# Performance work log

Hardware: AMD Instinct MI355X
Metric: run time of the kernel (lower is better)

## Reference

```python
import jax, jax.numpy as jnp
import numpy as np

# PyTorch LSTM gate order: i, f, g, o. Biases b_ih+b_hh combined into one b.

def _lstm(x, Wih, Whh, b, reverse=False):
    # x: [T, B, D] time-major; Wih: [4H, D]; Whh: [4H, H]; b: [4H]
    H = Whh.shape[1]
    B = x.shape[1]
    xi = jnp.einsum('tbd,gd->tbg', x, Wih) + b  # precompute input projection over all timesteps
    def step(carry, xt):
        h, c = carry
        z = xt + h @ Whh.T
        i, f, g, o = jnp.split(z, 4, axis=-1)
        c = jax.nn.sigmoid(f) * c + jax.nn.sigmoid(i) * jnp.tanh(g)
        h = jax.nn.sigmoid(o) * jnp.tanh(c)
        return (h, c), h
    h0 = jnp.zeros((B, H), x.dtype)
    _, hs = jax.lax.scan(step, (h0, h0), xi, reverse=reverse)
    return hs  # [T, B, H], aligned with input time indices


def _bidir(x, wf, wr):
    # wf/wr = (Wih, Whh, b) for forward / reverse directions
    hf = _lstm(x, *wf, reverse=False)
    hr = _lstm(x, *wr, reverse=True)
    return jnp.concatenate([hf, hr], axis=-1)


def setup_inputs() -> dict:
    key = jax.random.key(0)
    ks = jax.random.split(key, 20)
    B, T, F = 1024, 512, 1
    H1, H2 = 64, 32
    s = 0.05
    def p(k, shape):
        return jax.random.normal(k, shape, dtype=jnp.float32) * s
    inp = {
        'x': jax.random.normal(ks[0], (B, T, F), dtype=jnp.float32),
        # layer 1 (input F -> H1), fwd + rev
        'wih1f': p(ks[1], (4 * H1, F)), 'whh1f': p(ks[2], (4 * H1, H1)), 'b1f': p(ks[3], (4 * H1,)),
        'wih1r': p(ks[4], (4 * H1, F)), 'whh1r': p(ks[5], (4 * H1, H1)), 'b1r': p(ks[6], (4 * H1,)),
        # layer 2 (input 2*H1 -> H2), fwd + rev
        'wih2f': p(ks[7], (4 * H2, 2 * H1)), 'whh2f': p(ks[8], (4 * H2, H2)), 'b2f': p(ks[9], (4 * H2,)),
        'wih2r': p(ks[10], (4 * H2, 2 * H1)), 'whh2r': p(ks[11], (4 * H2, H2)), 'b2r': p(ks[12], (4 * H2,)),
        # MLP head
        'w_fc1': p(ks[13], (64, 2 * H2)), 'b_fc1': p(ks[14], (64,)),
        'w_out': p(ks[15], (1, 64)), 'b_out': p(ks[16], (1,)),
    }
    return inp


def reference(x, wih1f, whh1f, b1f, wih1r, whh1r, b1r,
              wih2f, whh2f, b2f, wih2r, whh2r, b2r,
              w_fc1, b_fc1, w_out, b_out):
    # Dropout layers act as identity in eval mode.
    xt = jnp.transpose(x, (1, 0, 2))  # [T, B, F]
    h1 = _bidir(xt, (wih1f, whh1f, b1f), (wih1r, whh1r, b1r))   # [T, B, 2*H1]
    h2 = _bidir(h1, (wih2f, whh2f, b2f), (wih2r, whh2r, b2r))   # [T, B, 2*H2]
    last = h2[-1]  # x[:, -1, :] in batch-first layout -> [B, 2*H2]
    z = jax.nn.relu(last @ w_fc1.T + b_fc1)
    return jax.nn.sigmoid(z @ w_out.T + b_out)[:, 0]  # [B]
```

## Files before the change

### kernel.cpp

```cpp
#include <hip/hip_runtime.h>
#include <hip/hip_bf16.h>
#include <math.h>

#define T_STEPS 512
#define BATCH   1024
#define NL2E    (-1.44269504f)

typedef __attribute__((ext_vector_type(8))) short short8;
typedef __attribute__((ext_vector_type(4))) float f32x4;

#define MFMA16(A, B, C) __builtin_amdgcn_mfma_f32_16x16x32_bf16((A), (B), (C), 0, 0, 0)

__device__ __forceinline__ void lds_barrier() {
    asm volatile("s_waitcnt lgkmcnt(0)" ::: "memory");
    __builtin_amdgcn_s_barrier();
}

__device__ __forceinline__ float psig(float zs) {
    return __builtin_amdgcn_rcpf(1.0f + __builtin_amdgcn_exp2f(zs));
}
__device__ __forceinline__ float ptanh(float zs) {
    return fmaf(2.0f, __builtin_amdgcn_rcpf(1.0f + __builtin_amdgcn_exp2f(zs)), -1.0f);
}
__device__ __forceinline__ float tanh_c(float c) {
    return fmaf(2.0f, __builtin_amdgcn_rcpf(
        1.0f + __builtin_amdgcn_exp2f(2.0f * NL2E * c)), -1.0f);
}
__device__ __forceinline__ unsigned short f2bf(float f) {
    unsigned int u = __float_as_uint(f);
    u += 0x7fffu + ((u >> 16) & 1u);
    return (unsigned short)(u >> 16);
}
__device__ __forceinline__ short8 ldfrag_lin_s(const float* __restrict__ p, float s) {
    short8 r;
#pragma unroll
    for (int e = 0; e < 8; ++e) r[e] = (short)f2bf(p[e] * s);
    return r;
}
__device__ __forceinline__ short8 ldfrag_s2_s(const float* __restrict__ p, int lg, float s) {
    short8 r;
#pragma unroll
    for (int e = 0; e < 8; ++e) r[e] = (short)f2bf(p[(e >> 2) * 16 + lg * 4 + (e & 3)] * s);
    return r;
}

__global__ __launch_bounds__(256, 1) void l1dual_kernel(
    const float* __restrict__ x,
    const float* __restrict__ whh1f, const float* __restrict__ wih1f, const float* __restrict__ b1f,
    const float* __restrict__ whh1r, const float* __restrict__ wih1r, const float* __restrict__ b1r,
    unsigned short* __restrict__ arch_f, unsigned short* __restrict__ arch_r)
{
    __shared__ __align__(16) float xT[T_STEPS][20];
    __shared__ __align__(16) short hT[2][16][72];

    const int blk = blockIdx.x;
    const int dir = blk & 1;
    const int tile = blk >> 1;
    const int tid = threadIdx.x;
    const int wv = tid >> 6, l = tid & 63, lg = l >> 4, lr = l & 15;

    const float* __restrict__ whh = dir ? whh1r : whh1f;
    const float* __restrict__ wih = dir ? wih1r : wih1f;
    const float* __restrict__ bbp = dir ? b1r : b1f;
    unsigned short* __restrict__ archb =
        (dir ? arch_r : arch_f) + (size_t)tile * T_STEPS * 16 * 64;

    for (int i = tid; i < T_STEPS * 16; i += 256) {
        const int b = i >> 9, t = i & 511;
        xT[t][b] = x[(size_t)(tile * 16 + b) * T_STEPS + t];
    }
    for (int i = tid; i < 2 * 16 * 72; i += 256) ((short*)hT)[i] = 0;

    short8 BW[8]; float wihv[4], bvv[4];
#pragma unroll
    for (int g = 0; g < 4; ++g) {
        const float sf = (g == 2) ? 2.0f * NL2E : NL2E;
        const int row = g * 64 + wv * 16 + lr;
        BW[2 * g]     = ldfrag_lin_s(whh + row * 64 + lg * 8, sf);
        BW[2 * g + 1] = ldfrag_lin_s(whh + row * 64 + 32 + lg * 8, sf);
        wihv[g] = wih[row] * sf; bvv[g] = bbp[row] * sf;
    }
    float cst[4] = {0.f, 0.f, 0.f, 0.f};
    __syncthreads();

    for (int i = 0; i < T_STEPS; ++i) {
        const int t = dir ? (T_STEPS - 1 - i) : i;
        const int rp = (t + 1) & 1;
        const short8 a0 = *(const short8*)&hT[rp][lr][lg * 8];
        const short8 a1 = *(const short8*)&hT[rp][lr][32 + lg * 8];
        f32x4 z[4];
#pragma unroll
        for (int g = 0; g < 4; ++g) {
            f32x4 za = {0.f, 0.f, 0.f, 0.f}, zb = {0.f, 0.f, 0.f, 0.f};
            za = MFMA16(a0, BW[2 * g], za);
            zb = MFMA16(a1, BW[2 * g + 1], zb);
            z[g] = za + zb;
        }
        const float4 x4v = *(const float4*)&xT[t][lg * 4];
        const float xa[4] = {x4v.x, x4v.y, x4v.z, x4v.w};
#pragma unroll
        for (int j = 0; j < 4; ++j) {
            const float vi = psig (z[0][j] + fmaf(xa[j], wihv[0], bvv[0]));
            const float vf = psig (z[1][j] + fmaf(xa[j], wihv[1], bvv[1]));
            const float vg = ptanh(z[2][j] + fmaf(xa[j], wihv[2], bvv[2]));
            const float vo = psig (z[3][j] + fmaf(xa[j], wihv[3], bvv[3]));
            cst[j] = fmaf(vf, cst[j], vi * vg);
            const float h = vo * tanh_c(cst[j]);
            const unsigned short hb = f2bf(h);
            hT[t & 1][lg * 4 + j][wv * 16 + lr] = (short)hb;
            archb[((size_t)t * 16 + lg * 4 + j) * 64 + wv * 16 + lr] = hb;
        }
        lds_barrier();
    }
}

__global__ __launch_bounds__(192, 1) void l2pc_kernel(
    const float* __restrict__ wih2f, const float* __restrict__ whh2f, const float* __restrict__ b2f,
    const float* __restrict__ wih2r, const float* __restrict__ b2r,
    const float* __restrict__ w_fc1, const float* __restrict__ b_fc1,
    const float* __restrict__ w_out, const float* __restrict__ b_out,
    const unsigned short* __restrict__ arch_f, const unsigned short* __restrict__ arch_r,
    float* __restrict__ out)
{
    __shared__ __align__(16) float4 zpreL[2][8][8][64];

    const int bt = blockIdx.x, tid = threadIdx.x;
    const int wv = tid >> 6, l = tid & 63, lg = l >> 4, lr = l & 15;
    const unsigned short* __restrict__ af = arch_f + (size_t)bt * T_STEPS * 16 * 64;
    const unsigned short* __restrict__ ar = arch_r + (size_t)bt * T_STEPS * 16 * 64;

    if (wv < 2) {
        short8 AF[4][4]; f32x4 bz[4];
#pragma unroll
        for (int mi = 0; mi < 4; ++mi) {
            const int m = wv * 4 + mi;
            const float sf = ((m >> 1) == 2) ? 2.0f * NL2E : NL2E;
            const int row = m * 16 + lr;
            AF[mi][0] = ldfrag_lin_s(wih2f + row * 128 + lg * 8, sf);
            AF[mi][1] = ldfrag_lin_s(wih2f + row * 128 + 32 + lg * 8, sf);
            AF[mi][2] = ldfrag_lin_s(wih2f + row * 128 + 64 + lg * 8, sf);
            AF[mi][3] = ldfrag_lin_s(wih2f + row * 128 + 96 + lg * 8, sf);
#pragma unroll
            for (int j = 0; j < 4; ++j) bz[mi][j] = b2f[m * 16 + 4 * lg + j] * sf;
        }
        auto FILL = [&](int cc) {
#pragma unroll 2
            for (int ss = 0; ss < 8; ++ss) {
                const int s = cc * 8 + ss;
                const size_t o = (size_t)(s * 16 + lr) * 64 + lg * 8;
                const short8 f0 = *(const short8*)(af + o);
                const short8 f1 = *(const short8*)(af + o + 32);
                const short8 r0 = *(const short8*)(ar + o);
                const short8 r1 = *(const short8*)(ar + o + 32);
#pragma unroll
                for (int mi = 0; mi < 4; ++mi) {
                    f32x4 a = bz[mi];
                    a = MFMA16(AF[mi][0], f0, a);
                    a = MFMA16(AF[mi][1], f1, a);
                    a = MFMA16(AF[mi][2], r0, a);
                    a = MFMA16(AF[mi][3], r1, a);
                    zpreL[cc & 1][ss][wv * 4 + mi][l] =
                        make_float4(a[0], a[1], a[2], a[3]);
                }
            }
        };
        FILL(0);
        lds_barrier();
        for (int c = 0; c < T_STEPS / 8; ++c) {
            if (c + 1 < T_STEPS / 8) FILL(c + 1);
            lds_barrier();
        }
    } else {
        short8 A2[8];
#pragma unroll
        for (int m = 0; m < 8; ++m) {
            const float sf = ((m >> 1) == 2) ? 2.0f * NL2E : NL2E;
            A2[m] = ldfrag_s2_s(whh2f + (m * 16 + lr) * 32, lg, sf);
        }
        short8 Bh2 = {0, 0, 0, 0, 0, 0, 0, 0};
        float c2[8];
#pragma unroll
        for (int i = 0; i < 8; ++i) c2[i] = 0.f;

        lds_barrier();
        for (int c = 0; c < T_STEPS / 8; ++c) {
#pragma unroll 2
            for (int ss = 0; ss < 8; ++ss) {
                f32x4 z[8];
#pragma unroll
                for (int m = 0; m < 8; ++m) {
                    const f32x4 zp = *(const f32x4*)&zpreL[c & 1][ss][m][l];
                    z[m] = MFMA16(A2[m], Bh2, zp);
                }
                unsigned short h2b[2][4];
#pragma unroll
                for (int uh = 0; uh < 2; ++uh) {
#pragma unroll
                    for (int j = 0; j < 4; ++j) {
                        const float vi = psig (z[uh][j]);
                        const float vf = psig (z[2 + uh][j]);
                        const float vg = ptanh(z[4 + uh][j]);
                        const float vo = psig (z[6 + uh][j]);
                        float& cc2 = c2[uh * 4 + j];
                        cc2 = fmaf(vf, cc2, vi * vg);
                        h2b[uh][j] = f2bf(vo * tanh_c(cc2));
                    }
                }
#pragma unroll
                for (int e = 0; e < 8; ++e) Bh2[e] = (short)h2b[e >> 2][e & 3];
            }
            lds_barrier();
        }

        short8 Bb = {0, 0, 0, 0, 0, 0, 0, 0};
        if (lg == 0) Bb[0] = (short)0x3F80;
        const size_t oL = (size_t)((T_STEPS - 1) * 16 + lr) * 64 + lg * 8;
        const short8 f0 = *(const short8*)(af + oL);
        const short8 f1 = *(const short8*)(af + oL + 32);
        const short8 r0 = *(const short8*)(ar + oL);
        const short8 r1 = *(const short8*)(ar + oL + 32);
        f32x4 ze[8];
#pragma unroll
        for (int mm = 0; mm < 8; ++mm) {
            const int row = mm * 16 + lr;
            const float sfe = ((mm >> 1) == 2) ? 2.0f * NL2E : NL2E;
            const short8 A0 = ldfrag_lin_s(wih2r + row * 128 + lg * 8, sfe);
            const short8 A1 = ldfrag_lin_s(wih2r + row * 128 + 32 + lg * 8, sfe);
            const short8 A2e = ldfrag_lin_s(wih2r + row * 128 + 64 + lg * 8, sfe);
            const short8 A3 = ldfrag_lin_s(wih2r + row * 128 + 96 + lg * 8, sfe);
            short8 bf = {0, 0, 0, 0, 0, 0, 0, 0};
            if (lg == 0) bf[0] = (short)f2bf(b2r[row] * sfe);
            f32x4 za = {0.f, 0.f, 0.f, 0.f}, zb = {0.f, 0.f, 0.f, 0.f};
            za = MFMA16(A0, f0, za);
            za = MFMA16(A2e, r0, za);
            za = MFMA16(bf, Bb, za);
            zb = MFMA16(A1, f1, zb);
            zb = MFMA16(A3, r1, zb);
            ze[mm] = za + zb;
        }
        short8 BR = {0, 0, 0, 0, 0, 0, 0, 0};
#pragma unroll
        for (int uh = 0; uh < 2; ++uh) {
#pragma unroll
            for (int j = 0; j < 4; ++j) {
                const float vi = psig (ze[uh][j]);
                const float vg = ptanh(ze[4 + uh][j]);
                const float vo = psig (ze[6 + uh][j]);
                BR[uh * 4 + j] = (short)f2bf(vo * tanh_c(vi * vg));
            }
        }
        float part = 0.f;
#pragma unroll
        for (int mm = 0; mm < 4; ++mm) {
            const int row = mm * 16 + lr;
            const short8 A0 = ldfrag_s2_s(w_fc1 + row * 64, lg, 1.0f);
            const short8 A1 = ldfrag_s2_s(w_fc1 + row * 64 + 32, lg, 1.0f);
            short8 bf = {0, 0, 0, 0, 0, 0, 0, 0};
            if (lg == 0) bf[0] = (short)f2bf(b_fc1[row]);
            f32x4 a = {0.f, 0.f, 0.f, 0.f};
            a = MFMA16(A0, Bh2, a);
            a = MFMA16(A1, BR, a);
            a = MFMA16(bf, Bb, a);
#pragma unroll
            for (int j = 0; j < 4; ++j)
                part += fmaxf(a[j], 0.f) * w_out[mm * 16 + lg * 4 + j];
        }
        part += __shfl_xor(part, 16, 64);
        part += __shfl_xor(part, 32, 64);
        if (l < 16) out[bt * 16 + lr] = psig(NL2E * (part + b_out[0]));
    }
}

extern "C" void kernel_launch(void* const* d_in, const int* in_sizes, int n_in,
                              void* d_out, int out_size, void* d_ws, size_t ws_size,
                              hipStream_t stream) {
    const float* x     = (const float*)d_in[0];
    const float* wih1f = (const float*)d_in[1];
    const float* whh1f = (const float*)d_in[2];
    const float* b1f   = (const float*)d_in[3];
    const float* wih1r = (const float*)d_in[4];
    const float* whh1r = (const float*)d_in[5];
    const float* b1r   = (const float*)d_in[6];
    const float* wih2f = (const float*)d_in[7];
    const float* whh2f = (const float*)d_in[8];
    const float* b2f   = (const float*)d_in[9];
    const float* wih2r = (const float*)d_in[10];
    const float* b2r   = (const float*)d_in[12];
    const float* w_fc1 = (const float*)d_in[13];
    const float* b_fc1 = (const float*)d_in[14];
    const float* w_out = (const float*)d_in[15];
    const float* b_out = (const float*)d_in[16];
    float* out = (float*)d_out;

    unsigned short* arch_f = (unsigned short*)d_ws;
    unsigned short* arch_r = arch_f + (size_t)64 * T_STEPS * 16 * 64;

    l1dual_kernel<<<dim3(128), dim3(256), 0, stream>>>(
        x, whh1f, wih1f, b1f, whh1r, wih1r, b1r, arch_f, arch_r);
    l2pc_kernel<<<dim3(64), dim3(192), 0, stream>>>(
        wih2f, whh2f, b2f, wih2r, b2r,
        w_fc1, b_fc1, w_out, b_out, arch_f, arch_r, out);
}
```

Before: 609.1 us.

## Split layer-2 recurrence across two wavefronts with LDS flag handshake

The layer-2 recurrent path used to run on one wavefront that computed all 8 gate tiles per step. It now runs on two wavefronts, each owning half of the hidden units (4 gate tiles). After every timestep the two exchange their bf16 hidden halves through a double-buffered LDS slot, using spin-wait flags. This halves the MFMA and activation work per wave on the serial critical path, but adds LDS round trips and a flag handshake with s_sleep at every one of the 512 steps.

```diff
diff --git a/kernel.cpp b/kernel.cpp
--- a/kernel.cpp
+++ b/kernel.cpp
@@ -114,7 +114,7 @@
     }
 }
 
-__global__ __launch_bounds__(192, 1) void l2pc_kernel(
+__global__ __launch_bounds__(256, 1) void l2pc_kernel(
     const float* __restrict__ wih2f, const float* __restrict__ whh2f, const float* __restrict__ b2f,
     const float* __restrict__ wih2r, const float* __restrict__ b2r,
     const float* __restrict__ w_fc1, const float* __restrict__ b_fc1,
@@ -123,11 +123,15 @@
     float* __restrict__ out)
 {
     __shared__ __align__(16) float4 zpreL[2][8][8][64];
+    __shared__ __align__(8)  uint2  exD[2][2][64];
+    __shared__ int exFlag[2];
 
     const int bt = blockIdx.x, tid = threadIdx.x;
     const int wv = tid >> 6, l = tid & 63, lg = l >> 4, lr = l & 15;
     const unsigned short* __restrict__ af = arch_f + (size_t)bt * T_STEPS * 16 * 64;
     const unsigned short* __restrict__ ar = arch_r + (size_t)bt * T_STEPS * 16 * 64;
+
+    if (tid < 2) exFlag[tid] = 0;
 
     if (wv < 2) {
         short8 AF[4][4]; f32x4 bz[4];
@@ -171,103 +175,121 @@
             lds_barrier();
         }
     } else {
-        short8 A2[8];
-#pragma unroll
-        for (int m = 0; m < 8; ++m) {
-            const float sf = ((m >> 1) == 2) ? 2.0f * NL2E : NL2E;
-            A2[m] = ldfrag_s2_s(whh2f + (m * 16 + lr) * 32, lg, sf);
+        const int cw = wv - 2;
+        short8 A2[4];
+#pragma unroll
+        for (int g = 0; g < 4; ++g) {
+            const int m = 2 * g + cw;
+            const float sf = (g == 2) ? 2.0f * NL2E : NL2E;
+            A2[g] = ldfrag_s2_s(whh2f + (m * 16 + lr) * 32, lg, sf);
         }
         short8 Bh2 = {0, 0, 0, 0, 0, 0, 0, 0};
-        float c2[8];
-#pragma unroll
-        for (int i = 0; i < 8; ++i) c2[i] = 0.f;
+        float c2[4] = {0.f, 0.f, 0.f, 0.f};
+        volatile int* myf = (volatile int*)&exFlag[cw];
+        volatile int* otf = (volatile int*)&exFlag[cw ^ 1];
 
         lds_barrier();
+        int s = 0;
         for (int c = 0; c < T_STEPS / 8; ++c) {
 #pragma unroll 2
-            for (int ss = 0; ss < 8; ++ss) {
-                f32x4 z[8];
-#pragma unroll
-                for (int m = 0; m < 8; ++m) {
-                    const f32x4 zp = *(const f32x4*)&zpreL[c & 1][ss][m][l];
-                    z[m] = MFMA16(A2[m], Bh2, zp);
+            for (int ss = 0; ss < 8; ++ss, ++s) {
+                f32x4 z[4];
+#pragma unroll
+                for (int g = 0; g < 4; ++g) {
+                    const f32x4 zp = *(const f32x4*)&zpreL[c & 1][ss][2 * g + cw][l];
+                    z[g] = MFMA16(A2[g], Bh2, zp);
                 }
-                unsigned short h2b[2][4];
-#pragma unroll
-                for (int uh = 0; uh < 2; ++uh) {
-#pragma unroll
-                    for (int j = 0; j < 4; ++j) {
-                        const float vi = psig (z[uh][j]);
-                        const float vf = psig (z[2 + uh][j]);
-                        const float vg = ptanh(z[4 + uh][j]);
-                        const float vo = psig (z[6 + uh][j]);
-                        float& cc2 = c2[uh * 4 + j];
-                        cc2 = fmaf(vf, cc2, vi * vg);
-                        h2b[uh][j] = f2bf(vo * tanh_c(cc2));
-                    }
+                unsigned short hb[4];
+#pragma unroll
+                for (int j = 0; j < 4; ++j) {
+                    const float vi = psig (z[0][j]);
+                    const float vf = psig (z[1][j]);
+                    const float vg = ptanh(z[2][j]);
+                    const float vo = psig (z[3][j]);
+                    c2[j] = fmaf(vf, c2[j], vi * vg);
+                    hb[j] = f2bf(vo * tanh_c(c2[j]));
                 }
-#pragma unroll
-                for (int e = 0; e < 8; ++e) Bh2[e] = (short)h2b[e >> 2][e & 3];
+                uint2 own;
+                own.x = (unsigned)hb[0] | ((unsigned)hb[1] << 16);
+                own.y = (unsigned)hb[2] | ((unsigned)hb[3] << 16);
+                exD[cw][s & 1][l] = own;
+                asm volatile("s_waitcnt lgkmcnt(0)" ::: "memory");
+                if (l == 0) *myf = s + 1;
+                while (*otf <= s) __builtin_amdgcn_s_sleep(1);
+                asm volatile("" ::: "memory");
+                const uint2 oth = exD[cw ^ 1][s & 1][l];
+                const uint2 lo = cw ? oth : own;
+                const uint2 hi = cw ? own : oth;
+                Bh2[0] = (short)(lo.x);
+                Bh2[1] = (short)(lo.x >> 16);
+                Bh2[2] = (short)(lo.y);
+                Bh2[3] = (short)(lo.y >> 16);
+                Bh2[4] = (short)(hi.x);
+                Bh2[5] = (short)(hi.x >> 16);
+                Bh2[6] = (short)(hi.y);
+                Bh2[7] = (short)(hi.y >> 16);
             }
             lds_barrier();
         }
 
-        short8 Bb = {0, 0, 0, 0, 0, 0, 0, 0};
-        if (lg == 0) Bb[0] = (short)0x3F80;
-        const size_t oL = (size_t)((T_STEPS - 1) * 16 + lr) * 64 + lg * 8;
-        const short8 f0 = *(const short8*)(af + oL);
-        const short8 f1 = *(const short8*)(af + oL + 32);
-        const short8 r0 = *(const short8*)(ar + oL);
-        const short8 r1 = *(const short8*)(ar + oL + 32);
-        f32x4 ze[8];
-#pragma unroll
-        for (int mm = 0; mm < 8; ++mm) {
-            const int row = mm * 16 + lr;
-            const float sfe = ((mm >> 1) == 2) ? 2.0f * NL2E : NL2E;
-            const short8 A0 = ldfrag_lin_s(wih2r + row * 128 + lg * 8, sfe);
-            const short8 A1 = ldfrag_lin_s(wih2r + row * 128 + 32 + lg * 8, sfe);
-            const short8 A2e = ldfrag_lin_s(wih2r + row * 128 + 64 + lg * 8, sfe);
-            const short8 A3 = ldfrag_lin_s(wih2r + row * 128 + 96 + lg * 8, sfe);
-            short8 bf = {0, 0, 0, 0, 0, 0, 0, 0};
-            if (lg == 0) bf[0] = (short)f2bf(b2r[row] * sfe);
-            f32x4 za = {0.f, 0.f, 0.f, 0.f}, zb = {0.f, 0.f, 0.f, 0.f};
-            za = MFMA16(A0, f0, za);
-            za = MFMA16(A2e, r0, za);
-            za = MFMA16(bf, Bb, za);
-            zb = MFMA16(A1, f1, zb);
-            zb = MFMA16(A3, r1, zb);
-            ze[mm] = za + zb;
-        }
-        short8 BR = {0, 0, 0, 0, 0, 0, 0, 0};
-#pragma unroll
-        for (int uh = 0; uh < 2; ++uh) {
-#pragma unroll
-            for (int j = 0; j < 4; ++j) {
-                const float vi = psig (ze[uh][j]);
-                const float vg = ptanh(ze[4 + uh][j]);
-                const float vo = psig (ze[6 + uh][j]);
-                BR[uh * 4 + j] = (short)f2bf(vo * tanh_c(vi * vg));
-            }
-        }
-        float part = 0.f;
-#pragma unroll
-        for (int mm = 0; mm < 4; ++mm) {
-            const int row = mm * 16 + lr;
-            const short8 A0 = ldfrag_s2_s(w_fc1 + row * 64, lg, 1.0f);
-            const short8 A1 = ldfrag_s2_s(w_fc1 + row * 64 + 32, lg, 1.0f);
-            short8 bf = {0, 0, 0, 0, 0, 0, 0, 0};
-            if (lg == 0) bf[0] = (short)f2bf(b_fc1[row]);
-            f32x4 a = {0.f, 0.f, 0.f, 0.f};
-            a = MFMA16(A0, Bh2, a);
-            a = MFMA16(A1, BR, a);
-            a = MFMA16(bf, Bb, a);
-#pragma unroll
-            for (int j = 0; j < 4; ++j)
-                part += fmaxf(a[j], 0.f) * w_out[mm * 16 + lg * 4 + j];
-        }
-        part += __shfl_xor(part, 16, 64);
-        part += __shfl_xor(part, 32, 64);
-        if (l < 16) out[bt * 16 + lr] = psig(NL2E * (part + b_out[0]));
+        if (cw == 0) {
+            short8 Bb = {0, 0, 0, 0, 0, 0, 0, 0};
+            if (lg == 0) Bb[0] = (short)0x3F80;
+            const size_t oL = (size_t)((T_STEPS - 1) * 16 + lr) * 64 + lg * 8;
+            const short8 f0 = *(const short8*)(af + oL);
+            const short8 f1 = *(const short8*)(af + oL + 32);
+            const short8 r0 = *(const short8*)(ar + oL);
+            const short8 r1 = *(const short8*)(ar + oL + 32);
+            f32x4 ze[8];
+#pragma unroll
+            for (int mm = 0; mm < 8; ++mm) {
+                const int row = mm * 16 + lr;
+                const float sfe = ((mm >> 1) == 2) ? 2.0f * NL2E : NL2E;
+                const short8 A0 = ldfrag_lin_s(wih2r + row * 128 + lg * 8, sfe);
+                const short8 A1 = ldfrag_lin_s(wih2r + row * 128 + 32 + lg * 8, sfe);
+                const short8 A2e = ldfrag_lin_s(wih2r + row * 128 + 64 + lg * 8, sfe);
+                const short8 A3 = ldfrag_lin_s(wih2r + row * 128 + 96 + lg * 8, sfe);
+                short8 bf = {0, 0, 0, 0, 0, 0, 0, 0};
+                if (lg == 0) bf[0] = (short)f2bf(b2r[row] * sfe);
+                f32x4 za = {0.f, 0.f, 0.f, 0.f}, zb = {0.f, 0.f, 0.f, 0.f};
+                za = MFMA16(A0, f0, za);
+                za = MFMA16(A2e, r0, za);
+                za = MFMA16(bf, Bb, za);
+                zb = MFMA16(A1, f1, zb);
+                zb = MFMA16(A3, r1, zb);
+                ze[mm] = za + zb;
+            }
+            short8 BR = {0, 0, 0, 0, 0, 0, 0, 0};
+#pragma unroll
+            for (int uh = 0; uh < 2; ++uh) {
+#pragma unroll
+                for (int j = 0; j < 4; ++j) {
+                    const float vi = psig (ze[uh][j]);
+                    const float vg = ptanh(ze[4 + uh][j]);
+                    const float vo = psig (ze[6 + uh][j]);
+                    BR[uh * 4 + j] = (short)f2bf(vo * tanh_c(vi * vg));
+                }
+            }
+            float part = 0.f;
+#pragma unroll
+            for (int mm = 0; mm < 4; ++mm) {
+                const int row = mm * 16 + lr;
+                const short8 A0 = ldfrag_s2_s(w_fc1 + row * 64, lg, 1.0f);
+                const short8 A1 = ldfrag_s2_s(w_fc1 + row * 64 + 32, lg, 1.0f);
+                short8 bf = {0, 0, 0, 0, 0, 0, 0, 0};
+                if (lg == 0) bf[0] = (short)f2bf(b_fc1[row]);
+                f32x4 a = {0.f, 0.f, 0.f, 0.f};
+                a = MFMA16(A0, Bh2, a);
+                a = MFMA16(A1, BR, a);
+                a = MFMA16(bf, Bb, a);
+#pragma unroll
+                for (int j = 0; j < 4; ++j)
+                    part += fmaxf(a[j], 0.f) * w_out[mm * 16 + lg * 4 + j];
+            }
+            part += __shfl_xor(part, 16, 64);
+            part += __shfl_xor(part, 32, 64);
+            if (l < 16) out[bt * 16 + lr] = psig(NL2E * (part + b_out[0]));
+        }
     }
 }
 
@@ -297,7 +319,7 @@
 
     l1dual_kernel<<<dim3(128), dim3(256), 0, stream>>>(
         x, whh1f, wih1f, b1f, whh1r, wih1r, b1r, arch_f, arch_r);
-    l2pc_kernel<<<dim3(64), dim3(192), 0, stream>>>(
+    l2pc_kernel<<<dim3(64), dim3(256), 0, stream>>>(
         wih2f, whh2f, b2f, wih2r, b2r,
         w_fc1, b_fc1, w_out, b_out, arch_f, arch_r, out);
 }
```

Result: faster. 550.2 us (-9.7%).
